# Performance work log

Measured on AMD Instinct MI355X. Metric: run time of the kernel, lower is better.

Reference implementation:

```python
import jax, jax.numpy as jnp
import numpy as np

GROUP_SIZE = 64
IN_F, OUT_F, RANK = 4096, 4096, 32
N_TOKENS = 4096
N_GROUPS = IN_F // GROUP_SIZE


def setup_inputs() -> dict:
    key = jax.random.key(0)
    k = jax.random.split(key, 6)
    x = jax.random.normal(k[0], (N_TOKENS, IN_F), dtype=jnp.float32)
    # signed int4 values in [-8, 7], stored unpacked as int32
    main_qweight = jax.random.randint(k[1], (OUT_F, N_GROUPS, GROUP_SIZE), -8, 8, dtype=jnp.int32)
    main_wscale = jax.random.uniform(k[2], (OUT_F, N_GROUPS), dtype=jnp.float32) * 0.02 + 1e-3
    bias = jax.random.normal(k[3], (OUT_F,), dtype=jnp.float32) * 0.02
    proj_down_dense = jax.random.normal(k[4], (IN_F, RANK), dtype=jnp.float32) * 0.02
    proj_up_dense = jax.random.normal(k[5], (RANK, OUT_F), dtype=jnp.float32) * 0.02
    return {
        "x": x,
        "main_qweight": main_qweight,
        "main_wscale": main_wscale,
        "bias": bias,
        "proj_down_dense": proj_down_dense,
        "proj_up_dense": proj_up_dense,
    }


def reference(x, main_qweight, main_wscale, bias, proj_down_dense, proj_up_dense):
    n = x.shape[0]
    # --- per-group int8 activation quantization (symmetric, max-abs/127) ---
    xg = x.reshape(n, N_GROUPS, GROUP_SIZE).astype(jnp.float32)  # [N, G, gs]
    max_abs = jnp.max(jnp.abs(xg), axis=-1, keepdims=True)
    ascale = jnp.where(max_abs > 0, max_abs * (1.0 / 127.0), jnp.ones_like(max_abs))
    qx = jnp.clip(jnp.round(xg / ascale), -127.0, 127.0)
    # Fold per-group activation scales back in; per (out, group) weight scales into weight.
    # out[n,o] = sum_g ascale[n,g] * wscale[o,g] * sum_k qx[n,g,k] * qw[o,g,k]
    a_deq = (qx * ascale).reshape(n, IN_F)                                   # [N, in]
    w_deq = (main_qweight.astype(jnp.float32) * main_wscale[..., None]).reshape(OUT_F, IN_F)  # [out, in]
    out = a_deq @ w_deq.T + bias.astype(jnp.float32)                          # [N, out], fp32 accumulate
    # --- SVD low-rank correction: x @ proj_down @ proj_up (down in x dtype, up in fp32) ---
    low_rank = x @ proj_down_dense                                            # [N, rank]
    out = out + low_rank.astype(jnp.float32) @ proj_up_dense.astype(jnp.float32)
    return out.astype(x.dtype)
```

## Files before the change

### kernel.cpp

```cpp
#include <hip/hip_runtime.h>
#include <hip/hip_bf16.h>

#define IN_F  4096
#define OUT_F 4096
#define NTOK  4096
#define RANK  32
#define GS    64
#define NG    64
#define KTOT  4160
#define KCH   1024

typedef __attribute__((ext_vector_type(4))) float f32x4;
typedef __attribute__((ext_vector_type(8))) short bf16x8;

__device__ __forceinline__ ushort f2bf(float f) {
  union { float f; uint u; } c; c.f = f;
  const uint u = c.u;
  return (ushort)((u + 0x7fffu + ((u >> 16) & 1u)) >> 16);
}

__global__ __launch_bounds__(256)
void quant_kernel(const float* __restrict__ x, ushort* __restrict__ Aext)
{
  const int tid  = threadIdx.x;
  const int wave = tid >> 6, lane = tid & 63;
  const int sub  = lane & 15;
  const int ggrp = blockIdx.x * 16 + wave * 4 + (lane >> 4);
  const int row  = ggrp >> 6, g = ggrp & 63;

  const float4 v = *(const float4*)(x + (size_t)row * IN_F + g * GS + sub * 4);
  float m = fmaxf(fmaxf(fabsf(v.x), fabsf(v.y)), fmaxf(fabsf(v.z), fabsf(v.w)));
  m = fmaxf(m, __shfl_xor(m, 1));
  m = fmaxf(m, __shfl_xor(m, 2));
  m = fmaxf(m, __shfl_xor(m, 4));
  m = fmaxf(m, __shfl_xor(m, 8));
  const float ascale = (m > 0.f) ? m * (1.f / 127.f) : 1.f;

  const float d0 = fminf(fmaxf(rintf(v.x / ascale), -127.f), 127.f) * ascale;
  const float d1 = fminf(fmaxf(rintf(v.y / ascale), -127.f), 127.f) * ascale;
  const float d2 = fminf(fmaxf(rintf(v.z / ascale), -127.f), 127.f) * ascale;
  const float d3 = fminf(fmaxf(rintf(v.w / ascale), -127.f), 127.f) * ascale;

  uint2 st;
  st.x = (uint)f2bf(d0) | ((uint)f2bf(d1) << 16);
  st.y = (uint)f2bf(d2) | ((uint)f2bf(d3) << 16);
  *(uint2*)(Aext + (size_t)row * KTOT + g * GS + sub * 4) = st;
}

__global__ __launch_bounds__(256)
void wdeq_kernel(const int* __restrict__ qw, const float* __restrict__ wsc,
                 ushort* __restrict__ Bext)
{
  const int gidx = blockIdx.x * 256 + threadIdx.x;
  const int o  = gidx >> 9;
  const int i0 = (gidx & 511) << 3;
  const float sc = wsc[o * NG + (i0 >> 6)];
  const int4 qa = *(const int4*)(qw + (size_t)o * IN_F + i0);
  const int4 qb = *(const int4*)(qw + (size_t)o * IN_F + i0 + 4);
  uint4 st;
  st.x = (uint)f2bf(qa.x * sc) | ((uint)f2bf(qa.y * sc) << 16);
  st.y = (uint)f2bf(qa.z * sc) | ((uint)f2bf(qa.w * sc) << 16);
  st.z = (uint)f2bf(qb.x * sc) | ((uint)f2bf(qb.y * sc) << 16);
  st.w = (uint)f2bf(qb.z * sc) | ((uint)f2bf(qb.w * sc) << 16);
  *(uint4*)(Bext + (size_t)o * KTOT + i0) = st;
}

__global__ __launch_bounds__(256)
void aux_kernel(const float* __restrict__ pd, const float* __restrict__ pu,
                ushort* __restrict__ Bext, ushort* __restrict__ pdT)
{
  const int id = blockIdx.x * 256 + threadIdx.x;
  ushort* dst = Bext + (size_t)id * KTOT + IN_F;
  #pragma unroll
  for (int r = 0; r < RANK; ++r) {
    dst[r]        = f2bf(pu[(size_t)r * OUT_F + id]);
    dst[RANK + r] = 0;
  }
  #pragma unroll
  for (int r = 0; r < RANK; ++r)
    pdT[(size_t)r * IN_F + id] = f2bf(pd[(size_t)id * RANK + r]);
}

__global__ __launch_bounds__(256)
void lr_kernel(const ushort* __restrict__ A, const ushort* __restrict__ pdT,
               float* __restrict__ part)
{
  __shared__ alignas(16) ushort lA[64 * 64];
  const int tid  = threadIdx.x;
  const int wave = tid >> 6, lane = tid & 63;
  const int mt = blockIdx.x >> 2;
  const int kc = blockIdx.x & 3;
  const int k0 = kc * KCH;

  const int tr  = tid >> 3;
  const int scc = (tid & 7) ^ (tr & 7);
  const ushort* aSrc = A + (size_t)(mt * 64 + tr) * KTOT + k0 + scc * 8;
  char* ldsA = (char*)lA + wave * 1024;

  f32x4 acc[2];
  #pragma unroll
  for (int n = 0; n < 2; ++n) acc[n] = f32x4{0.f, 0.f, 0.f, 0.f};

  for (int kt = 0; kt < KCH / 64; ++kt) {
    const ushort* aS = aSrc + kt * 64;
    #pragma unroll
    for (int j = 0; j < 2; ++j)
      __builtin_amdgcn_global_load_lds(
          (const __attribute__((address_space(1))) void*)(aS + (size_t)j * 32 * KTOT),
          (__attribute__((address_space(3))) void*)(ldsA + j * 4096), 16, 0, 0);
    __syncthreads();
    #pragma unroll
    for (int ks = 0; ks < 2; ++ks) {
      const int kb  = (ks * 32 + (lane >> 4) * 8) * 2;
      const int row = wave * 16 + (lane & 15);
      const int addr = (row * 128 + kb) ^ ((row & 7) << 4);
      bf16x8 af = *(const bf16x8*)((const char*)lA + addr);
      #pragma unroll
      for (int n = 0; n < 2; ++n) {
        const int prow = n * 16 + (lane & 15);
        bf16x8 bf = *(const bf16x8*)(pdT + (size_t)prow * IN_F + k0 + kt * 64 + ks * 32 + (lane >> 4) * 8);
        acc[n] = __builtin_amdgcn_mfma_f32_16x16x32_bf16(af, bf, acc[n], 0, 0, 0);
      }
    }
    __syncthreads();
  }
  const int r0   = lane & 15;
  const int rowb = mt * 64 + wave * 16 + (lane >> 4) * 4;
  #pragma unroll
  for (int n = 0; n < 2; ++n)
    #pragma unroll
    for (int i = 0; i < 4; ++i)
      part[((size_t)kc * 4096 + rowb + i) * 32 + n * 16 + r0] = acc[n][i];
}

__global__ __launch_bounds__(256)
void lrcomb_kernel(const float* __restrict__ part, ushort* __restrict__ Aext)
{
  const int id  = blockIdx.x * 256 + threadIdx.x;
  const int row = id >> 5, r = id & 31;
  const float s = part[(size_t)row * 32 + r]
                + part[(size_t)(4096 + row) * 32 + r]
                + part[(size_t)(8192 + row) * 32 + r]
                + part[(size_t)(12288 + row) * 32 + r];
  Aext[(size_t)row * KTOT + IN_F + r]        = f2bf(s);
  Aext[(size_t)row * KTOT + IN_F + RANK + r] = 0;
}

__global__ __launch_bounds__(256, 2)
void gemm_kernel(const ushort* __restrict__ A, const ushort* __restrict__ B,
                 const float* __restrict__ bias, float* __restrict__ C)
{
  __shared__ alignas(16) ushort lA[128 * 64];
  __shared__ alignas(16) ushort lB[128 * 64];
  const int tid  = threadIdx.x;
  const int wave = tid >> 6, lane = tid & 63;
  const int wg = (blockIdx.x & 7) * 128 + (blockIdx.x >> 3);
  const int bm = wg >> 5, bn = wg & 31;
  const int wm = wave >> 1, wn = wave & 1;

  const int tr  = tid >> 3;
  const int scc = (tid & 7) ^ (tr & 7);
  const ushort* aSrc = A + (size_t)(bm * 128 + tr) * KTOT + scc * 8;
  const ushort* bSrc = B + (size_t)(bn * 128 + tr) * KTOT + scc * 8;
  char* ldsA = (char*)lA + wave * 1024;
  char* ldsB = (char*)lB + wave * 1024;

  f32x4 acc[4][4];
  #pragma unroll
  for (int m = 0; m < 4; ++m)
    #pragma unroll
    for (int n = 0; n < 4; ++n)
      acc[m][n] = f32x4{0.f, 0.f, 0.f, 0.f};

  for (int kt = 0; kt < KTOT / 64; ++kt) {
    const ushort* aS = aSrc + kt * 64;
    const ushort* bS = bSrc + kt * 64;
    #pragma unroll
    for (int j = 0; j < 4; ++j)
      __builtin_amdgcn_global_load_lds(
          (const __attribute__((address_space(1))) void*)(aS + (size_t)j * 32 * KTOT),
          (__attribute__((address_space(3))) void*)(ldsA + j * 4096), 16, 0, 0);
    #pragma unroll
    for (int j = 0; j < 4; ++j)
      __builtin_amdgcn_global_load_lds(
          (const __attribute__((address_space(1))) void*)(bS + (size_t)j * 32 * KTOT),
          (__attribute__((address_space(3))) void*)(ldsB + j * 4096), 16, 0, 0);
    __syncthreads();

    #pragma unroll
    for (int ks = 0; ks < 2; ++ks) {
      const int kb = (ks * 32 + (lane >> 4) * 8) * 2;
      bf16x8 af[4], bfr[4];
      #pragma unroll
      for (int m = 0; m < 4; ++m) {
        const int row  = wm * 64 + m * 16 + (lane & 15);
        const int addr = (row * 128 + kb) ^ ((row & 7) << 4);
        af[m] = *(const bf16x8*)((const char*)lA + addr);
      }
      #pragma unroll
      for (int n = 0; n < 4; ++n) {
        const int row  = wn * 64 + n * 16 + (lane & 15);
        const int addr = (row * 128 + kb) ^ ((row & 7) << 4);
        bfr[n] = *(const bf16x8*)((const char*)lB + addr);
      }
      #pragma unroll
      for (int m = 0; m < 4; ++m)
        #pragma unroll
        for (int n = 0; n < 4; ++n)
          acc[m][n] = __builtin_amdgcn_mfma_f32_16x16x32_bf16(af[m], bfr[n], acc[m][n], 0, 0, 0);
    }
    __syncthreads();
  }

  const int col0  = bn * 128 + wn * 64 + (lane & 15);
  const int rbase = bm * 128 + wm * 64 + (lane >> 4) * 4;
  #pragma unroll
  for (int n = 0; n < 4; ++n) {
    const float bv = bias[col0 + n * 16];
    #pragma unroll
    for (int m = 0; m < 4; ++m) {
      #pragma unroll
      for (int i = 0; i < 4; ++i)
        C[(size_t)(rbase + m * 16 + i) * OUT_F + col0 + n * 16] = acc[m][n][i] + bv;
    }
  }
}

extern "C" void kernel_launch(void* const* d_in, const int* in_sizes, int n_in,
                              void* d_out, int out_size, void* d_ws, size_t ws_size,
                              hipStream_t stream) {
  const float* x    = (const float*)d_in[0];
  const int*   qw   = (const int*)d_in[1];
  const float* wsc  = (const float*)d_in[2];
  const float* bias = (const float*)d_in[3];
  const float* pd   = (const float*)d_in[4];
  const float* pu   = (const float*)d_in[5];
  float* out = (float*)d_out;

  ushort* Aext = (ushort*)d_ws;
  ushort* Bext = Aext + (size_t)NTOK * KTOT;
  ushort* pdT  = Bext + (size_t)OUT_F * KTOT;
  float*  part = (float*)(pdT + (size_t)RANK * IN_F);

  quant_kernel <<<16384, 256, 0, stream>>>(x, Aext);
  wdeq_kernel  <<< 8192, 256, 0, stream>>>(qw, wsc, Bext);
  aux_kernel   <<<   16, 256, 0, stream>>>(pd, pu, Bext, pdT);
  lr_kernel    <<<  256, 256, 0, stream>>>(Aext, pdT, part);
  lrcomb_kernel<<<  512, 256, 0, stream>>>(part, Aext);
  gemm_kernel  <<< 1024, 256, 0, stream>>>(Aext, Bext, bias, out);
}
```

Before: 203.1 us.

## Replace GEMM with 256x256-tile, double-buffered, phase-pipelined kernel

Swaps the 128x128 single-buffered bf16 GEMM for a 256x256-tile kernel using 512 threads and 128KB of dynamic LDS. The LDS is double-buffered, and the work is split into eight phases per iteration, so global-to-LDS loads for later k-tiles run during MFMA work on the current ones. It also uses s_setprio around the MFMA blocks and a custom XCD-aware block-to-tile mapping. K is padded from 4160 to 4224 to give an even number of k-tiles, which adds a little extra zero work and workspace, and only one block fits per CU.

```diff
diff --git a/kernel.cpp b/kernel.cpp
--- a/kernel.cpp
+++ b/kernel.cpp
@@ -7,7 +7,9 @@
 #define RANK  32
 #define GS    64
 #define NG    64
-#define KTOT  4160
+#define KTOT  4224
+#define NKT   66
+#define ITERS 33
 #define KCH   1024
 
 typedef __attribute__((ext_vector_type(4))) float f32x4;
@@ -73,8 +75,10 @@
   ushort* dst = Bext + (size_t)id * KTOT + IN_F;
   #pragma unroll
   for (int r = 0; r < RANK; ++r) {
-    dst[r]        = f2bf(pu[(size_t)r * OUT_F + id]);
-    dst[RANK + r] = 0;
+    dst[r]            = f2bf(pu[(size_t)r * OUT_F + id]);
+    dst[RANK + r]     = 0;
+    dst[2 * RANK + r] = 0;
+    dst[3 * RANK + r] = 0;
   }
   #pragma unroll
   for (int r = 0; r < RANK; ++r)
@@ -142,86 +146,143 @@
                 + part[(size_t)(4096 + row) * 32 + r]
                 + part[(size_t)(8192 + row) * 32 + r]
                 + part[(size_t)(12288 + row) * 32 + r];
-  Aext[(size_t)row * KTOT + IN_F + r]        = f2bf(s);
-  Aext[(size_t)row * KTOT + IN_F + RANK + r] = 0;
-}
-
-__global__ __launch_bounds__(256, 2)
-void gemm_kernel(const ushort* __restrict__ A, const ushort* __restrict__ B,
-                 const float* __restrict__ bias, float* __restrict__ C)
-{
-  __shared__ alignas(16) ushort lA[128 * 64];
-  __shared__ alignas(16) ushort lB[128 * 64];
-  const int tid  = threadIdx.x;
-  const int wave = tid >> 6, lane = tid & 63;
-  const int wg = (blockIdx.x & 7) * 128 + (blockIdx.x >> 3);
-  const int bm = wg >> 5, bn = wg & 31;
-  const int wm = wave >> 1, wn = wave & 1;
-
-  const int tr  = tid >> 3;
-  const int scc = (tid & 7) ^ (tr & 7);
-  const ushort* aSrc = A + (size_t)(bm * 128 + tr) * KTOT + scc * 8;
-  const ushort* bSrc = B + (size_t)(bn * 128 + tr) * KTOT + scc * 8;
-  char* ldsA = (char*)lA + wave * 1024;
-  char* ldsB = (char*)lB + wave * 1024;
-
-  f32x4 acc[4][4];
-  #pragma unroll
-  for (int m = 0; m < 4; ++m)
+  ushort* dst = Aext + (size_t)row * KTOT + IN_F;
+  dst[r]            = f2bf(s);
+  dst[RANK + r]     = 0;
+  dst[2 * RANK + r] = 0;
+  dst[3 * RANK + r] = 0;
+}
+
+__device__ __forceinline__ void stageA(const ushort* __restrict__ Atile, char* lds,
+                                       int b, int h, int kt, int w, int lane)
+{
+  #pragma unroll
+  for (int l = 0; l < 2; ++l) {
+    const int g = w * 2 + l;
+    const int quarter = h + (g >> 3) * 2;
+    const int sub = g & 7;
+    const int grow = quarter * 64 + sub * 8 + (lane >> 3);
+    const ushort* src = Atile + (size_t)grow * KTOT + kt * 64 + (((lane & 7) ^ (lane >> 3)) << 3);
+    __builtin_amdgcn_global_load_lds(
+        (const __attribute__((address_space(1))) void*)src,
+        (__attribute__((address_space(3))) void*)(lds + b * 32768 + quarter * 8192 + sub * 1024),
+        16, 0, 0);
+  }
+}
+
+__device__ __forceinline__ void stageB(const ushort* __restrict__ Btile, char* lds,
+                                       int b, int h, int kt, int w, int lane)
+{
+  #pragma unroll
+  for (int l = 0; l < 2; ++l) {
+    const int g = w * 2 + l;
+    const int j = g >> 2;
+    const int sub = g & 3;
+    const int grow = j * 64 + h * 32 + sub * 8 + (lane >> 3);
+    const ushort* src = Btile + (size_t)grow * KTOT + kt * 64 + (((lane & 7) ^ (lane >> 3)) << 3);
+    __builtin_amdgcn_global_load_lds(
+        (const __attribute__((address_space(1))) void*)src,
+        (__attribute__((address_space(3))) void*)(lds + 65536 + b * 32768 + j * 8192 + h * 4096 + sub * 1024),
+        16, 0, 0);
+  }
+}
+
+#define PHASE(B_, MQ_, NQ_, STAGE, WAIT4)                                        \
+  {                                                                              \
+    bf16x8 af[4][2], bfm[2][2];                                                  \
+    const int aqb = (B_) * 32768 + (wm * 2 + (MQ_)) * 8192;                      \
+    const int bqb = 65536 + (B_) * 32768 + wn * 8192;                            \
+    _Pragma("unroll")                                                            \
+    for (int mf = 0; mf < 4; ++mf) {                                             \
+      const int r = mf * 16 + l15;                                               \
+      _Pragma("unroll")                                                          \
+      for (int ks = 0; ks < 2; ++ks)                                             \
+        af[mf][ks] = *(const bf16x8*)(lds + aqb + (((r * 128) + kbyte[ks]) ^ ((r & 7) << 4))); \
+    }                                                                            \
+    _Pragma("unroll")                                                            \
+    for (int nf = 0; nf < 2; ++nf) {                                             \
+      const int r = ((NQ_) * 2 + nf) * 16 + l15;                                 \
+      _Pragma("unroll")                                                          \
+      for (int ks = 0; ks < 2; ++ks)                                             \
+        bfm[nf][ks] = *(const bf16x8*)(lds + bqb + (((r * 128) + kbyte[ks]) ^ ((r & 7) << 4))); \
+    }                                                                            \
+    STAGE;                                                                       \
+    __builtin_amdgcn_s_barrier();                                                \
+    __builtin_amdgcn_s_setprio(1);                                               \
+    _Pragma("unroll")                                                            \
+    for (int mf = 0; mf < 4; ++mf)                                               \
+      _Pragma("unroll")                                                          \
+      for (int nf = 0; nf < 2; ++nf)                                             \
+        _Pragma("unroll")                                                        \
+        for (int ks = 0; ks < 2; ++ks)                                           \
+          acc[(MQ_) * 4 + mf][(NQ_) * 2 + nf] =                                  \
+              __builtin_amdgcn_mfma_f32_16x16x32_bf16(af[mf][ks], bfm[nf][ks],   \
+                  acc[(MQ_) * 4 + mf][(NQ_) * 2 + nf], 0, 0, 0);                 \
+    __builtin_amdgcn_s_setprio(0);                                               \
+    if (WAIT4) asm volatile("s_waitcnt vmcnt(4)" ::: "memory");                  \
+    __builtin_amdgcn_s_barrier();                                                \
+  }
+
+__global__ __launch_bounds__(512, 2)
+void gemm256_kernel(const ushort* __restrict__ A, const ushort* __restrict__ B,
+                    const float* __restrict__ bias, float* __restrict__ C)
+{
+  extern __shared__ char lds[];
+  const int tid = threadIdx.x;
+  const int w = tid >> 6, lane = tid & 63;
+  const int l15 = lane & 15;
+  const int wm = w >> 2, wn = w & 3;
+  int kbyte[2];
+  kbyte[0] = ((lane >> 4) * 8) * 2;
+  kbyte[1] = (32 + (lane >> 4) * 8) * 2;
+
+  const int xcd = blockIdx.x & 7, idx = blockIdx.x >> 3;
+  const int bm = (xcd >> 1) * 4 + (idx >> 3);
+  const int bn = (xcd & 1) * 8 + (idx & 7);
+
+  const ushort* Atile = A + (size_t)bm * 256 * KTOT;
+  const ushort* Btile = B + (size_t)bn * 256 * KTOT;
+
+  f32x4 acc[8][4];
+  #pragma unroll
+  for (int m = 0; m < 8; ++m)
     #pragma unroll
     for (int n = 0; n < 4; ++n)
       acc[m][n] = f32x4{0.f, 0.f, 0.f, 0.f};
 
-  for (int kt = 0; kt < KTOT / 64; ++kt) {
-    const ushort* aS = aSrc + kt * 64;
-    const ushort* bS = bSrc + kt * 64;
-    #pragma unroll
-    for (int j = 0; j < 4; ++j)
-      __builtin_amdgcn_global_load_lds(
-          (const __attribute__((address_space(1))) void*)(aS + (size_t)j * 32 * KTOT),
-          (__attribute__((address_space(3))) void*)(ldsA + j * 4096), 16, 0, 0);
-    #pragma unroll
-    for (int j = 0; j < 4; ++j)
-      __builtin_amdgcn_global_load_lds(
-          (const __attribute__((address_space(1))) void*)(bS + (size_t)j * 32 * KTOT),
-          (__attribute__((address_space(3))) void*)(ldsB + j * 4096), 16, 0, 0);
-    __syncthreads();
-
-    #pragma unroll
-    for (int ks = 0; ks < 2; ++ks) {
-      const int kb = (ks * 32 + (lane >> 4) * 8) * 2;
-      bf16x8 af[4], bfr[4];
-      #pragma unroll
-      for (int m = 0; m < 4; ++m) {
-        const int row  = wm * 64 + m * 16 + (lane & 15);
-        const int addr = (row * 128 + kb) ^ ((row & 7) << 4);
-        af[m] = *(const bf16x8*)((const char*)lA + addr);
-      }
-      #pragma unroll
-      for (int n = 0; n < 4; ++n) {
-        const int row  = wn * 64 + n * 16 + (lane & 15);
-        const int addr = (row * 128 + kb) ^ ((row & 7) << 4);
-        bfr[n] = *(const bf16x8*)((const char*)lB + addr);
-      }
-      #pragma unroll
-      for (int m = 0; m < 4; ++m)
-        #pragma unroll
-        for (int n = 0; n < 4; ++n)
-          acc[m][n] = __builtin_amdgcn_mfma_f32_16x16x32_bf16(af[m], bfr[n], acc[m][n], 0, 0, 0);
-    }
-    __syncthreads();
-  }
-
-  const int col0  = bn * 128 + wn * 64 + (lane & 15);
-  const int rbase = bm * 128 + wm * 64 + (lane >> 4) * 4;
-  #pragma unroll
-  for (int n = 0; n < 4; ++n) {
-    const float bv = bias[col0 + n * 16];
-    #pragma unroll
-    for (int m = 0; m < 4; ++m) {
+  stageA(Atile, lds, 0, 0, 0, w, lane);
+  stageB(Btile, lds, 0, 0, 0, w, lane);
+  stageB(Btile, lds, 0, 1, 0, w, lane);
+  stageA(Atile, lds, 0, 1, 0, w, lane);
+  stageA(Atile, lds, 1, 0, 1, w, lane);
+  stageB(Btile, lds, 1, 0, 1, w, lane);
+  asm volatile("s_waitcnt vmcnt(4)" ::: "memory");
+  __builtin_amdgcn_s_barrier();
+
+  #pragma unroll 1
+  for (int j = 0; j < ITERS; ++j) {
+    const int t1 = 2 * j + 1, t2 = 2 * j + 2, t3 = 2 * j + 3;
+    PHASE(0, 0, 0, { stageB(Btile, lds, 1, 1, t1, w, lane); }, 0)
+    PHASE(0, 0, 1, { stageA(Atile, lds, 1, 1, t1, w, lane); }, 0)
+    PHASE(0, 1, 0, { if (t2 < NKT) stageA(Atile, lds, 0, 0, t2, w, lane); }, 0)
+    PHASE(0, 1, 1, { if (t2 < NKT) stageB(Btile, lds, 0, 0, t2, w, lane); }, 1)
+    PHASE(1, 0, 0, { if (t2 < NKT) stageB(Btile, lds, 0, 1, t2, w, lane); }, 0)
+    PHASE(1, 0, 1, { if (t2 < NKT) stageA(Atile, lds, 0, 1, t2, w, lane); }, 0)
+    PHASE(1, 1, 0, { if (t3 < NKT) stageA(Atile, lds, 1, 0, t3, w, lane); }, 0)
+    PHASE(1, 1, 1, { if (t3 < NKT) stageB(Btile, lds, 1, 0, t3, w, lane); }, 1)
+  }
+
+  const int csub = lane >> 4;
+  #pragma unroll
+  for (int nf = 0; nf < 4; ++nf) {
+    const int col = bn * 256 + wn * 64 + nf * 16 + l15;
+    const float bv = bias[col];
+    #pragma unroll
+    for (int mf = 0; mf < 8; ++mf) {
+      const int row = bm * 256 + wm * 128 + mf * 16 + csub * 4;
       #pragma unroll
       for (int i = 0; i < 4; ++i)
-        C[(size_t)(rbase + m * 16 + i) * OUT_F + col0 + n * 16] = acc[m][n][i] + bv;
+        C[(size_t)(row + i) * OUT_F + col] = acc[mf][nf][i] + bv;
     }
   }
 }
@@ -242,10 +303,13 @@
   ushort* pdT  = Bext + (size_t)OUT_F * KTOT;
   float*  part = (float*)(pdT + (size_t)RANK * IN_F);
 
+  hipFuncSetAttribute(reinterpret_cast<const void*>(gemm256_kernel),
+                      hipFuncAttributeMaxDynamicSharedMemorySize, 131072);
+
   quant_kernel <<<16384, 256, 0, stream>>>(x, Aext);
   wdeq_kernel  <<< 8192, 256, 0, stream>>>(qw, wsc, Bext);
   aux_kernel   <<<   16, 256, 0, stream>>>(pd, pu, Bext, pdT);
   lr_kernel    <<<  256, 256, 0, stream>>>(Aext, pdT, part);
   lrcomb_kernel<<<  512, 256, 0, stream>>>(part, Aext);
-  gemm_kernel  <<< 1024, 256, 0, stream>>>(Aext, Bext, bias, out);
-}
+  gemm256_kernel<<< 256, 512, 131072, stream>>>(Aext, Bext, bias, out);
+}
```

Measured after the change: 202.2 us. Within noise of the previous version (-0.4%).
